# Optimization experiments

Hardware: AMD Instinct MI355X
Metric: run time of the kernel (lower is better)

## Reference

```python
import jax, jax.numpy as jnp
import numpy as np

B, N, DIM, H = 8, 4096, 768, 12
HD = DIM // H
SCALE = HD ** -0.5


def setup_inputs() -> dict:
    key = jax.random.key(0)
    ks = jax.random.split(key, 6)
    x = jax.random.normal(ks[0], (B, N, DIM), dtype=jnp.float32)
    # torch nn.Linear weights: [out_features, in_features]
    Wqkv = jax.random.normal(ks[1], (3 * DIM, DIM), dtype=jnp.float32) * (DIM ** -0.5)
    Wp = jax.random.normal(ks[2], (DIM, DIM), dtype=jnp.float32) * (DIM ** -0.5)
    bp = jnp.zeros((DIM,), dtype=jnp.float32)
    w_q = jax.random.normal(ks[3], (H, HD), dtype=jnp.float32)
    w_k = jax.random.normal(ks[4], (H, HD), dtype=jnp.float32)
    return {"x": x, "Wqkv": Wqkv, "Wp": Wp, "bp": bp, "w_q": w_q, "w_k": w_k}


def reference(x, Wqkv, Wp, bp, w_q, w_k):
    b, n, c = x.shape
    qkv = x @ Wqkv.T                                   # [B,N,3C]
    # rearrange 'B N (qkv H C) -> qkv B H N C'
    qkv = qkv.reshape(b, n, 3, H, HD).transpose(2, 0, 3, 1, 4)
    q, k, v = qkv[0], qkv[1], qkv[2]                   # each [B,H,N,hd]

    alpha = jnp.einsum('bhnc,hc->bhn', q, w_q) * SCALE
    alpha = jax.nn.softmax(alpha, axis=-1)             # [B,H,N]
    global_q = jnp.einsum('bhn,bhnc->bhc', alpha, q)   # [B,H,hd]

    p = global_q[:, :, None, :] * k                    # [B,H,N,hd]
    beta = jnp.einsum('bhnc,hc->bhn', p, w_k) * SCALE
    beta = jax.nn.softmax(beta, axis=-1)
    global_k = jnp.einsum('bhn,bhnc->bhc', beta, k)    # [B,H,hd]

    u = global_k[:, :, None, :] * v                    # [B,H,N,hd]
    q_flat = q.transpose(0, 2, 1, 3).reshape(b, n, c)  # 'B H N C -> B N (H C)'
    u_flat = u.transpose(0, 2, 1, 3).reshape(b, n, c)
    return u_flat @ Wp.T + bp + q_flat
```

## Files before the change

kernel.cpp:

```cpp
#include <hip/hip_runtime.h>
#include <hip/hip_bf16.h>
#include <cstdint>
#include <cstddef>

#define B_ 8
#define N_ 4096
#define DIM_ 768
#define H_ 12
#define M_ (B_*N_)
#define SCALE_ 0.125f
#define NS2 16
#define KDIM 768
#define NKT 12
#define NITER 6

typedef __attribute__((ext_vector_type(8))) short s8v;
typedef __attribute__((ext_vector_type(4))) float f4v;

__device__ inline float bf2f(unsigned short u) {
    unsigned v = ((unsigned)u) << 16;
    return __builtin_bit_cast(float, v);
}
__device__ inline unsigned short f2bf(float f) {
    unsigned u = __builtin_bit_cast(unsigned, f);
    return (unsigned short)((u + 0x7FFFu + ((u >> 16) & 1u)) >> 16);
}
__device__ inline void gload16(const void* g, void* l) {
    __builtin_amdgcn_global_load_lds(
        (const __attribute__((address_space(1))) void*)g,
        (__attribute__((address_space(3))) void*)l, 16, 0, 0);
}

#define BARX() __builtin_amdgcn_s_barrier()
#define PRIO1() __builtin_amdgcn_s_setprio(1)
#define PRIO0() __builtin_amdgcn_s_setprio(0)
#define VM4() asm volatile("s_waitcnt vmcnt(4)" ::: "memory")
#define VM0() asm volatile("s_waitcnt vmcnt(0)" ::: "memory")

__global__ __launch_bounds__(512, 2)
void gemm8(const unsigned short* __restrict__ A, int ldaE,
           const unsigned short* __restrict__ Bmat,
           unsigned short* __restrict__ Cb,
           const unsigned short* __restrict__ avecb,
           float* __restrict__ pv1, float* __restrict__ pms1,
           int ntn)
{
    __shared__ __align__(16) char smem[131072];
    const int tid = threadIdx.x;
    const int l = tid & 63, w = tid >> 6;
    const int lr = l & 15, g = l >> 4;
    const int wm = w >> 2, wn = w & 3;

    const int nwg = gridDim.x, cpx = nwg >> 3;
    const int bid = blockIdx.x;
    const int lg = (bid & 7) * cpx + (bid >> 3);
    const int tm = lg / ntn, tn = lg % ntn;
    const int m0 = tm * 256, n0 = tn * 256;

    const long ldaB = (long)ldaE * 2;
    const long ldbB = (long)KDIM * 2;

    const int srA = w * 8 + (l >> 3);
    const int kbs = (l & 7) * 16;
    const int kbx = kbs ^ ((srA & 7) << 4);
    long offA[2], offB[2];
    offA[0] = (long)(srA) * ldaB + kbx;
    offA[1] = (long)(128 + srA) * ldaB + kbx;
    offB[0] = (long)(((srA >> 5)) * 64 + (srA & 31)) * ldbB + kbx;
    offB[1] = (long)((2 + (srA >> 5)) * 64 + (srA & 31)) * ldbB + kbx;

    const char* Abase = (const char*)(A + (size_t)m0 * ldaE);
    const char* Bbase = (const char*)(Bmat + (size_t)n0 * KDIM);

    const int aoff = (wm * 64 + lr) * 128;
    const int boff = (wn * 32 + lr) * 128;
    const int kx0 = (g * 16) ^ ((lr & 7) << 4);
    const int kx1 = (64 + g * 16) ^ ((lr & 7) << 4);

#define STG_A(buf_, qm_, kt_) { \
    const char* s0_ = Abase + (long)(kt_) * 2 + (long)(qm_) * 64 * ldaB; \
    char* d0_ = smem + ((buf_) * 4 + (qm_)) * 16384 + w * 1024; \
    gload16(s0_ + offA[0], d0_); \
    gload16(s0_ + offA[1], d0_ + 8192); }

#define STG_B(buf_, qn_, kt_) { \
    const char* s0_ = Bbase + (long)(kt_) * 2 + (long)(qn_) * 32 * ldbB; \
    char* d0_ = smem + ((buf_) * 4 + 2 + (qn_)) * 16384 + w * 1024; \
    gload16(s0_ + offB[0], d0_); \
    gload16(s0_ + offB[1], d0_ + 8192); }

    if (tn < 3) {
        f4v acc[8][4] = {};
        s8v af[4][2];
        s8v bfr[2][2][2];

#define DS_A(buf_, qm_) { \
    const char* ba_ = smem + ((buf_) * 4 + (qm_)) * 16384 + aoff; \
    af[0][0] = *(const s8v*)(ba_ +    0 + kx0); af[0][1] = *(const s8v*)(ba_ +    0 + kx1); \
    af[1][0] = *(const s8v*)(ba_ + 2048 + kx0); af[1][1] = *(const s8v*)(ba_ + 2048 + kx1); \
    af[2][0] = *(const s8v*)(ba_ + 4096 + kx0); af[2][1] = *(const s8v*)(ba_ + 4096 + kx1); \
    af[3][0] = *(const s8v*)(ba_ + 6144 + kx0); af[3][1] = *(const s8v*)(ba_ + 6144 + kx1); }

#define DS_B(buf_, qn_) { \
    const char* bb_ = smem + ((buf_) * 4 + 2 + (qn_)) * 16384 + boff; \
    bfr[qn_][0][0] = *(const s8v*)(bb_ +    0 + kx0); bfr[qn_][0][1] = *(const s8v*)(bb_ +    0 + kx1); \
    bfr[qn_][1][0] = *(const s8v*)(bb_ + 2048 + kx0); bfr[qn_][1][1] = *(const s8v*)(bb_ + 2048 + kx1); }

#define MM(fmg_, fng_, qn_, kk_) \
    acc[fmg_][fng_] = __builtin_amdgcn_mfma_f32_16x16x32_bf16(af[(fmg_)&3][kk_], bfr[qn_][(fng_)&1][kk_], acc[fmg_][fng_], 0, 0, 0);

#define MFMA8(qm_, qn_, kk_) \
    MM((qm_)*4+0, (qn_)*2+0, qn_, kk_) MM((qm_)*4+0, (qn_)*2+1, qn_, kk_) \
    MM((qm_)*4+1, (qn_)*2+0, qn_, kk_) MM((qm_)*4+1, (qn_)*2+1, qn_, kk_) \
    MM((qm_)*4+2, (qn_)*2+0, qn_, kk_) MM((qm_)*4+2, (qn_)*2+1, qn_, kk_) \
    MM((qm_)*4+3, (qn_)*2+0, qn_, kk_) MM((qm_)*4+3, (qn_)*2+1, qn_, kk_)

#define MFMA16(qm_, qn_) { MFMA8(qm_, qn_, 0) MFMA8(qm_, qn_, 1) }

        STG_A(0, 0, 0); STG_B(0, 0, 0); STG_A(0, 1, 0); STG_B(0, 1, 0);
        STG_A(1, 0, 64); STG_B(1, 0, 64);
        VM4(); BARX();

        for (int i = 0; i < NITER; ++i) {
            const int t1k = (2 * i + 1) * 64, t2k = (2 * i + 2) * 64, t3k = (2 * i + 3) * 64;
            const bool h2 = (2 * i + 2) < NKT, h3 = (2 * i + 3) < NKT;
            const bool last = (i == NITER - 1);
            DS_A(0, 0); DS_B(0, 0); STG_B(1, 1, t1k);
            BARX(); PRIO1(); MFMA16(0, 0); PRIO0(); BARX();
            DS_B(0, 1); STG_A(1, 1, t1k);
            BARX(); PRIO1(); MFMA16(0, 1); PRIO0(); BARX();
            DS_A(0, 1); if (h2) STG_A(0, 0, t2k);
            BARX(); PRIO1(); MFMA16(1, 0); PRIO0(); BARX();
            if (h2) STG_B(0, 0, t2k);
            BARX(); PRIO1(); MFMA16(1, 1); PRIO0();
            if (last) { VM0(); } else { VM4(); }
            BARX();
            DS_A(1, 0); DS_B(1, 0); if (h2) STG_A(0, 1, t2k);
            BARX(); PRIO1(); MFMA16(0, 0); PRIO0(); BARX();
            DS_B(1, 1); if (h2) STG_B(0, 1, t2k);
            BARX(); PRIO1(); MFMA16(0, 1); PRIO0(); BARX();
            DS_A(1, 1); if (h3) STG_A(1, 0, t3k);
            BARX(); PRIO1(); MFMA16(1, 0); PRIO0(); BARX();
            if (h3) STG_B(1, 0, t3k);
            BARX(); PRIO1(); MFMA16(1, 1); PRIO0();
            if (last) { VM0(); } else { VM4(); }
            BARX();
        }

        const int c0 = tn * 256;
#pragma unroll
        for (int fmg = 0; fmg < 8; ++fmg) {
#pragma unroll
            for (int fng = 0; fng < 4; ++fng) {
                const int col = c0 + wn * 64 + fng * 16 + lr;
#pragma unroll
                for (int r = 0; r < 4; ++r) {
                    const int row = m0 + wm * 128 + fmg * 16 + g * 4 + r;
                    Cb[(size_t)row * DIM_ + col] = f2bf(acc[fmg][fng][r]);
                }
            }
        }
#undef DS_A
#undef DS_B
#undef MM
#undef MFMA8
#undef MFMA16
    } else {
        const int b = m0 >> 12;
        const int slice = (m0 & (N_ - 1)) >> 8;
        if (w < 2) {
            const int rw = l >> 3;
            const int by = ((l & 7) * 16) ^ (rw << 4);
#pragma unroll
            for (int k6 = 0; k6 < 6; ++k6) {
                const int kt = w * 6 + k6;
                gload16((const char*)avecb + (size_t)rw * 1536 + kt * 128 + by,
                        smem + 32768 + kt * 2048);
                gload16((const char*)avecb + (size_t)(8 + rw) * 1536 + kt * 128 + by,
                        smem + 32768 + kt * 2048 + 1024);
            }
        }
        STG_A(0, 0, 0); STG_A(0, 1, 0);
        STG_A(1, 0, 64); STG_A(1, 1, 64);
        VM4(); BARX();

        f4v sacc[2] = {};
        for (int kt = 0; kt < 12; ++kt) {
            const int buf = kt & 1;
#pragma unroll
            for (int j = 0; j < 2; ++j) {
                const int r0 = w * 32 + j * 16;
                const int qm = (r0 >> 6) & 1, hi = r0 >> 7, loc = r0 & 63;
                const char* ab = smem + (buf * 4 + qm) * 16384 + hi * 8192 + (loc + lr) * 128;
                s8v a0 = *(const s8v*)(ab + kx0);
                s8v a1 = *(const s8v*)(ab + kx1);
                const char* vb = smem + 32768 + kt * 2048 + lr * 128;
                s8v b0 = *(const s8v*)(vb + kx0);
                s8v b1 = *(const s8v*)(vb + kx1);
                sacc[j] = __builtin_amdgcn_mfma_f32_16x16x32_bf16(a0, b0, sacc[j], 0, 0, 0);
                sacc[j] = __builtin_amdgcn_mfma_f32_16x16x32_bf16(a1, b1, sacc[j], 0, 0, 0);
            }
            BARX();
            if (kt + 2 < 12) {
                const int kk2 = (kt + 2) * 64;
                STG_A(buf, 0, kk2); STG_A(buf, 1, kk2);
            }
            if (kt <= 9) { VM4(); } else { VM0(); }
            BARX();
        }

        float dd[8];
#pragma unroll
        for (int j = 0; j < 2; ++j)
#pragma unroll
            for (int r = 0; r < 4; ++r) dd[j * 4 + r] = sacc[j][r] * SCALE_;

        float mw = dd[0];
#pragma unroll
        for (int q2 = 1; q2 < 8; ++q2) mw = fmaxf(mw, dd[q2]);
        mw = fmaxf(mw, __shfl_xor(mw, 16));
        mw = fmaxf(mw, __shfl_xor(mw, 32));
        float* Lm = (float*)(smem + 107008);
        float* Ls = (float*)(smem + 107520);
        if (l < 16) Lm[w * 16 + lr] = mw;
        __syncthreads();
        float mfin = Lm[lr];
#pragma unroll
        for (int w2 = 1; w2 < 8; ++w2) mfin = fmaxf(mfin, Lm[w2 * 16 + lr]);

        float ss = 0.f;
#pragma unroll
        for (int j = 0; j < 2; ++j)
#pragma unroll
            for (int r = 0; r < 4; ++r) {
                const float e = __expf(dd[j * 4 + r] - mfin);
                ss += e;
                const int row = w * 32 + j * 16 + g * 4 + r;
                *(unsigned short*)(smem + 98304 + lr * 544 + row * 2) = f2bf(e);
            }
        ss += __shfl_xor(ss, 16);
        ss += __shfl_xor(ss, 32);
        if (l < 16) Ls[w * 16 + lr] = ss;
        __syncthreads();

        if (tid < 12) {
            float S = 0.f;
#pragma unroll
            for (int w2 = 0; w2 < 8; ++w2) S += Ls[w2 * 16 + tid];
            float M2 = Lm[tid];
#pragma unroll
            for (int w2 = 1; w2 < 8; ++w2) M2 = fmaxf(M2, Lm[w2 * 16 + tid]);
            pms1[((size_t)(b * H_ + tid) * 16 + slice) * 2 + 0] = M2;
            pms1[((size_t)(b * H_ + tid) * 16 + slice) * 2 + 1] = S;
        }
        __syncthreads();

        for (int it = 0; it < 6; ++it) {
            const int ktA = it * 2, ktB = it * 2 + 1;
            STG_A(0, 0, ktA * 64); STG_A(0, 1, ktA * 64);
            STG_A(1, 0, ktB * 64); STG_A(1, 1, ktB * 64);
            VM0(); BARX();
            const int buf = w >> 2;
            const int kt = it * 2 + buf;
            const int d0 = (w & 3) * 16;
            const int dby = (d0 + (l & 15)) * 2;
            f4v pacc = {};
#pragma unroll
            for (int c = 0; c < 8; ++c) {
                s8v ae = *(const s8v*)(smem + 98304 + (l & 15) * 544
                                       + (c * 32 + (l >> 4) * 8) * 2);
                const char* xr = smem + (buf * 4 + ((c >> 1) & 1)) * 16384 + (c >> 2) * 8192;
                const int nb = (c & 1) * 32 + (l >> 4) * 8;
                s8v bx;
#pragma unroll
                for (int j = 0; j < 8; ++j)
                    bx[j] = (short)*(const unsigned short*)(xr + (nb + j) * 128 + (dby ^ (j << 4)));
                pacc = __builtin_amdgcn_mfma_f32_16x16x32_bf16(ae, bx, pacc, 0, 0, 0);
            }
            if ((l >> 4) < 3) {
#pragma unroll
                for (int r = 0; r < 4; ++r) {
                    const int h = (l >> 4) * 4 + r;
                    pv1[((size_t)(b * 16 + slice) * 12 + h) * 768
                        + kt * 64 + d0 + (l & 15)] = pacc[r];
                }
            }
            BARX();
        }
    }
#undef STG_A
#undef STG_B
}

template<int MODE>
__global__ __launch_bounds__(512, 2)
void gemm128(const unsigned short* __restrict__ A, int ldaE,
             const unsigned short* __restrict__ Bmat,
             float* __restrict__ Cf, unsigned short* __restrict__ CbO,
             const float* __restrict__ bias, const float* __restrict__ addW,
             int Nc, int ntn)
{
    __shared__ __align__(16) char smem[98304];
    const int tid = threadIdx.x;
    const int l = tid & 63, w = tid >> 6;
    const int lr = l & 15, g = l >> 4;
    const int wm = w >> 2, wn = w & 3;

    const int nwg = gridDim.x, cpx = nwg >> 3;
    const int bid = blockIdx.x;
    const int lg = (bid & 7) * cpx + (bid >> 3);
    const int tm = lg / ntn, tn = lg % ntn;
    const int m0 = tm * 128, n0 = tn * 256;

    const long ldaB = (long)ldaE * 2;
    const long ldbB = (long)KDIM * 2;

    const unsigned short* Bp = Bmat;
    if (MODE == 0) Bp = Bmat + (size_t)(m0 >> 12) * (DIM_ * DIM_);

    const int srA = w * 8 + (l >> 3);
    const int kbs = (l & 7) * 16;
    const int kbx = kbs ^ ((srA & 7) << 4);
    long offA[2], offB[2];
    offA[0] = (long)(srA) * ldaB + kbx;
    offA[1] = (long)(64 + srA) * ldaB + kbx;
    offB[0] = (long)(((srA >> 5)) * 64 + (srA & 31)) * ldbB + kbx;
    offB[1] = (long)((2 + (srA >> 5)) * 64 + (srA & 31)) * ldbB + kbx;

    const char* Abase = (const char*)(A + (size_t)m0 * ldaE);
    const char* Bbase = (const char*)(Bp + (size_t)n0 * KDIM);

    const int aoff = (wm * 64 + lr) * 128;
    const int boff = (wn * 32 + lr) * 128;
    const int kx0 = (g * 16) ^ ((lr & 7) << 4);
    const int kx1 = (64 + g * 16) ^ ((lr & 7) << 4);

    f4v acc[4][4] = {};
    s8v af[4][2];
    s8v bfr[2][2][2];

#define STG_A1(buf_, kt_) { \
    const char* s0_ = Abase + (long)(kt_) * 2; \
    char* d0_ = smem + ((buf_) * 3) * 16384 + w * 1024; \
    gload16(s0_ + offA[0], d0_); \
    gload16(s0_ + offA[1], d0_ + 8192); }

#define STG_B1(buf_, qn_, kt_) { \
    const char* s0_ = Bbase + (long)(kt_) * 2 + (long)(qn_) * 32 * ldbB; \
    char* d0_ = smem + ((buf_) * 3 + 1 + (qn_)) * 16384 + w * 1024; \
    gload16(s0_ + offB[0], d0_); \
    gload16(s0_ + offB[1], d0_ + 8192); }

#define DS_A1(buf_) { \
    const char* ba_ = smem + ((buf_) * 3) * 16384 + aoff; \
    af[0][0] = *(const s8v*)(ba_ +    0 + kx0); af[0][1] = *(const s8v*)(ba_ +    0 + kx1); \
    af[1][0] = *(const s8v*)(ba_ + 2048 + kx0); af[1][1] = *(const s8v*)(ba_ + 2048 + kx1); \
    af[2][0] = *(const s8v*)(ba_ + 4096 + kx0); af[2][1] = *(const s8v*)(ba_ + 4096 + kx1); \
    af[3][0] = *(const s8v*)(ba_ + 6144 + kx0); af[3][1] = *(const s8v*)(ba_ + 6144 + kx1); }

#define DS_B1(buf_, qn_) { \
    const char* bb_ = smem + ((buf_) * 3 + 1 + (qn_)) * 16384 + boff; \
    bfr[qn_][0][0] = *(const s8v*)(bb_ +    0 + kx0); bfr[qn_][0][1] = *(const s8v*)(bb_ +    0 + kx1); \
    bfr[qn_][1][0] = *(const s8v*)(bb_ + 2048 + kx0); bfr[qn_][1][1] = *(const s8v*)(bb_ + 2048 + kx1); }

#define MM1(fm_, fng_, qn_, kk_) \
    acc[fm_][fng_] = __builtin_amdgcn_mfma_f32_16x16x32_bf16(af[fm_][kk_], bfr[qn_][(fng_)&1][kk_], acc[fm_][fng_], 0, 0, 0);

#define MFMA16_1(qn_, kk_) \
    MM1(0, (qn_)*2+0, qn_, kk_) MM1(0, (qn_)*2+1, qn_, kk_) \
    MM1(1, (qn_)*2+0, qn_, kk_) MM1(1, (qn_)*2+1, qn_, kk_) \
    MM1(2, (qn_)*2+0, qn_, kk_) MM1(2, (qn_)*2+1, qn_, kk_) \
    MM1(3, (qn_)*2+0, qn_, kk_) MM1(3, (qn_)*2+1, qn_, kk_)

#define MFMA32_1(qn_) { MFMA16_1(qn_, 0) MFMA16_1(qn_, 1) }

    STG_A1(0, 0); STG_B1(0, 0, 0); STG_B1(0, 1, 0);
    STG_A1(1, 64); STG_B1(1, 0, 64);
    VM4(); BARX();

    for (int i = 0; i < NITER; ++i) {
        const int t1k = (2 * i + 1) * 64, t2k = (2 * i + 2) * 64, t3k = (2 * i + 3) * 64;
        const bool h2 = (2 * i + 2) < NKT, h3 = (2 * i + 3) < NKT;
        const bool last = (i == NITER - 1);
        DS_A1(0); DS_B1(0, 0); STG_B1(1, 1, t1k);
        BARX(); PRIO1(); MFMA32_1(0); PRIO0(); BARX();
        DS_B1(0, 1); if (h2) { STG_A1(0, t2k); STG_B1(0, 0, t2k); }
        BARX(); PRIO1(); MFMA32_1(1); PRIO0();
        if (last) { VM0(); } else { VM4(); }
        BARX();
        DS_A1(1); DS_B1(1, 0); if (h2) STG_B1(0, 1, t2k);
        BARX(); PRIO1(); MFMA32_1(0); PRIO0(); BARX();
        DS_B1(1, 1); if (h3) { STG_A1(1, t3k); STG_B1(1, 0, t3k); }
        BARX(); PRIO1(); MFMA32_1(1); PRIO0();
        if (last) { VM0(); } else { VM4(); }
        BARX();
    }

    const int jb = m0 % DIM_;
#pragma unroll
    for (int fm = 0; fm < 4; ++fm) {
#pragma unroll
        for (int fng = 0; fng < 4; ++fng) {
            const int col = n0 + wn * 64 + fng * 16 + lr;
#pragma unroll
            for (int r = 0; r < 4; ++r) {
                const int ro = wm * 64 + fm * 16 + g * 4 + r;
                const int row = m0 + ro;
                if (MODE == 0) {
                    Cf[(size_t)row * Nc + col] = acc[fm][fng][r] + bias[col];
                } else {
                    CbO[(size_t)row * Nc + col] =
                        f2bf(acc[fm][fng][r] + addW[(size_t)(jb + ro) * DIM_ + col]);
                }
            }
        }
    }
#undef STG_A1
#undef STG_B1
#undef DS_A1
#undef DS_B1
#undef MM1
#undef MFMA16_1
#undef MFMA32_1
}

__global__ __launch_bounds__(256)
void reduce_a(const float* __restrict__ pv1, const float* __restrict__ pms1,
              const float* __restrict__ Wqkv, const float* __restrict__ w_k,
              float* __restrict__ gqwk)
{
    const int b = blockIdx.x / H_, h = blockIdx.x % H_;
    const int t = threadIdx.x;
    const int w = t >> 6, l = t & 63;
    __shared__ float Svec[768];
    __shared__ float ew[16];
    __shared__ float Ssh;

    const float* pp = pms1 + (size_t)(b * H_ + h) * 16 * 2;
    float M = pp[0];
    for (int s = 1; s < 16; ++s) M = fmaxf(M, pp[s * 2]);
    if (t < 16) ew[t] = __expf(pp[t * 2] - M);
    __syncthreads();
    if (t == 0) {
        float S = 0.f;
        for (int s = 0; s < 16; ++s) S += ew[s] * pp[s * 2 + 1];
        Ssh = S;
    }
#pragma unroll
    for (int j = 0; j < 3; ++j) {
        const int col = t + j * 256;
        float v = 0.f;
        for (int s = 0; s < 16; ++s)
            v += ew[s] * pv1[((size_t)(b * 16 + s) * 12 + h) * 768 + col];
        Svec[col] = v;
    }
    __syncthreads();

    const float invS = 1.f / Ssh;
    for (int i = 0; i < 16; ++i) {
        const int o = w * 16 + i;
        const float* wr = Wqkv + (size_t)(h * 64 + o) * 768;
        float s = 0.f;
#pragma unroll
        for (int j = 0; j < 12; ++j)
            s += wr[l + j * 64] * Svec[l + j * 64];
        s += __shfl_xor(s, 1); s += __shfl_xor(s, 2); s += __shfl_xor(s, 4);
        s += __shfl_xor(s, 8); s += __shfl_xor(s, 16); s += __shfl_xor(s, 32);
        if (l == 0)
            gqwk[(size_t)(b * H_ + h) * 64 + o] = (s * invS) * w_k[h * 64 + o];
    }
}

__global__ __launch_bounds__(256)
void fused_b(const unsigned short* __restrict__ kb,
             const float* __restrict__ gqwk,
             float* __restrict__ pv2, float* __restrict__ pms2)
{
    const int bid = blockIdx.x;
    const int bh = bid / NS2, sp = bid % NS2;
    const int b = bh / H_, h = bh % H_;
    const int t = threadIdx.x;
    const int lane8 = t & 7, grp = t >> 3;

    __shared__ float gq_s[64];
    if (t < 64) gq_s[t] = gqwk[(size_t)bh * 64 + t];
    __syncthreads();

    float w8[8];
#pragma unroll
    for (int j = 0; j < 8; j++) w8[j] = gq_s[lane8 * 8 + j];

    const unsigned short* base = kb + ((size_t)(b * N_ + sp * 256) * DIM_)
                                 + h * 64 + lane8 * 8;
    float q[8][8];
    float d[8];
#pragma unroll
    for (int pass = 0; pass < 8; ++pass) {
        const int row = pass * 32 + grp;
        s8v q8 = *(const s8v*)(base + (size_t)row * DIM_);
        float s = 0.f;
#pragma unroll
        for (int j = 0; j < 8; j++) {
            q[pass][j] = bf2f((unsigned short)q8[j]);
            s += q[pass][j] * w8[j];
        }
        s += __shfl_xor(s, 1); s += __shfl_xor(s, 2); s += __shfl_xor(s, 4);
        d[pass] = s * SCALE_;
    }
    float m = d[0];
#pragma unroll
    for (int pass = 1; pass < 8; ++pass) m = fmaxf(m, d[pass]);
    float ssum = 0.f;
    float a8[8] = {};
#pragma unroll
    for (int pass = 0; pass < 8; ++pass) {
        float e = __expf(d[pass] - m);
        ssum += e;
#pragma unroll
        for (int j = 0; j < 8; j++) a8[j] += e * q[pass][j];
    }

    __shared__ float Lm[32], Ls[32];
    __shared__ float La[32][64];
    if (lane8 == 0) { Lm[grp] = m; Ls[grp] = ssum; }
#pragma unroll
    for (int j = 0; j < 8; j++) La[grp][lane8 * 8 + j] = a8[j];
    __syncthreads();

    if (t < 64) {
        float mstar = Lm[0];
#pragma unroll
        for (int g2 = 1; g2 < 32; ++g2) mstar = fmaxf(mstar, Lm[g2]);
        float sstar = 0.f, v = 0.f;
#pragma unroll
        for (int g2 = 0; g2 < 32; ++g2) {
            float e = __expf(Lm[g2] - mstar);
            sstar += Ls[g2] * e;
            v += La[g2][t] * e;
        }
        pv2[(size_t)bid * 64 + t] = v;
        if (t == 0) { pms2[bid * 2] = mstar; pms2[bid * 2 + 1] = sstar; }
    }
}

__global__ void path_reduce(const float* __restrict__ partv, const float* __restrict__ partms,
                            int nsp, float* __restrict__ gout)
{
    const int bh = blockIdx.x;
    const int t = threadIdx.x;
    float mstar = partms[(bh * nsp) * 2];
    for (int p = 1; p < nsp; ++p) mstar = fmaxf(mstar, partms[(bh * nsp + p) * 2]);
    float sstar = 0.f, v = 0.f;
    for (int p = 0; p < nsp; ++p) {
        float e = __expf(partms[(bh * nsp + p) * 2] - mstar);
        sstar += partms[(bh * nsp + p) * 2 + 1] * e;
        v += partv[(size_t)(bh * nsp + p) * 64 + t] * e;
    }
    gout[bh * 64 + t] = v / sstar;
}

__global__ __launch_bounds__(256)
void avec_prep(const float* __restrict__ Wqkv, const float* __restrict__ w_q,
               unsigned short* __restrict__ avecb)
{
    const int h = blockIdx.x;
    const int t = threadIdx.x;
    if (h >= H_) {
#pragma unroll
        for (int j = 0; j < 3; ++j) avecb[(size_t)h * 768 + t + j * 256] = 0;
        return;
    }
    __shared__ float wl[64];
    if (t < 64) wl[t] = w_q[h * 64 + t];
    __syncthreads();
#pragma unroll
    for (int j = 0; j < 3; ++j) {
        const int dcol = t + j * 256;
        float a = 0.f;
        for (int c = 0; c < 64; ++c)
            a += wl[c] * Wqkv[(size_t)(h * 64 + c) * 768 + dcol];
        avecb[(size_t)h * 768 + dcol] = f2bf(a);
    }
}

__global__ void cvt_all(const float* __restrict__ x, const float* __restrict__ Wqkv,
                        unsigned short* __restrict__ xb, unsigned short* __restrict__ wqkb,
                        unsigned short* __restrict__ wvT,
                        int n4x, int n4xw)
{
    int i = blockIdx.x * 256 + threadIdx.x;
    if (i < n4xw) {
        const float* src; unsigned short* dst; int k;
        if (i < n4x) { src = x; dst = xb; k = i; }
        else { src = Wqkv + (size_t)DIM_ * DIM_; dst = wqkb; k = i - n4x; }
        float4 v = ((const float4*)src)[k];
        ushort4 o;
        o.x = f2bf(v.x); o.y = f2bf(v.y); o.z = f2bf(v.z); o.w = f2bf(v.w);
        ((ushort4*)dst)[k] = o;
    } else {
        const int k = i - n4xw;
        const int ii = k % DIM_;
        const int c0 = (k / DIM_) * 4;
        ushort4 o;
        o.x = f2bf(Wqkv[(size_t)(2 * DIM_ + c0 + 0) * DIM_ + ii]);
        o.y = f2bf(Wqkv[(size_t)(2 * DIM_ + c0 + 1) * DIM_ + ii]);
        o.z = f2bf(Wqkv[(size_t)(2 * DIM_ + c0 + 2) * DIM_ + ii]);
        o.w = f2bf(Wqkv[(size_t)(2 * DIM_ + c0 + 3) * DIM_ + ii]);
        *(ushort4*)&wvT[(size_t)ii * DIM_ + c0] = o;
    }
}

__global__ __launch_bounds__(256)
void fold_wp(const float* __restrict__ Wp, const float* __restrict__ gk,
             unsigned short* __restrict__ W2)
{
    int idx = blockIdx.x * 256 + threadIdx.x;
    int e4 = idx * 4;
    int b = (int)((unsigned)e4 / (unsigned)(DIM_ * DIM_));
    int rem = e4 - b * (DIM_ * DIM_);
    int c = rem % DIM_;
    float4 wv = *(const float4*)&Wp[rem];
    const float* gp = &gk[b * DIM_ + c];
    ushort4 o;
    o.x = f2bf(wv.x * gp[0]); o.y = f2bf(wv.y * gp[1]);
    o.z = f2bf(wv.z * gp[2]); o.w = f2bf(wv.w * gp[3]);
    *(ushort4*)&W2[e4] = o;
}

extern "C" void kernel_launch(void* const* d_in, const int* in_sizes, int n_in,
                              void* d_out, int out_size, void* d_ws, size_t ws_size,
                              hipStream_t stream)
{
    const float* x    = (const float*)d_in[0];
    const float* Wqkv = (const float*)d_in[1];
    const float* Wp   = (const float*)d_in[2];
    const float* bp   = (const float*)d_in[3];
    const float* w_q  = (const float*)d_in[4];
    const float* w_k  = (const float*)d_in[5];
    float* out = (float*)d_out;

    constexpr size_t NXB = (size_t)M_ * DIM_;
    constexpr size_t NWK = (size_t)DIM_ * DIM_;
    constexpr size_t NWV = (size_t)DIM_ * DIM_;
    constexpr size_t NKB = (size_t)M_ * DIM_;
    constexpr size_t NW2 = (size_t)B_ * DIM_ * DIM_;

    char* p = (char*)d_ws;
    unsigned short* xb    = (unsigned short*)p; p += NXB * 2;
    unsigned short* wqkb  = (unsigned short*)p; p += NWK * 2;
    unsigned short* wvT   = (unsigned short*)p; p += NWV * 2;
    unsigned short* kb    = (unsigned short*)p; p += NKB * 2;
    unsigned short* w2b   = (unsigned short*)p; p += NW2 * 2;
    unsigned short* w4b   = (unsigned short*)p; p += NW2 * 2;
    unsigned short* avecb = (unsigned short*)p; p += (size_t)16 * 768 * 2;
    float* pv1  = (float*)p; p += (size_t)B_ * 16 * 12 * 768 * 4;
    float* pms1 = (float*)p; p += (size_t)B_ * H_ * 16 * 2 * 4;
    float* pv2  = (float*)p; p += (size_t)B_ * H_ * NS2 * 64 * 4;
    float* pms2 = (float*)p; p += (size_t)B_ * H_ * NS2 * 2 * 4;
    float* gqwk = (float*)p; p += (size_t)B_ * H_ * 64 * 4;
    float* gkv  = (float*)p; p += (size_t)B_ * H_ * 64 * 4;

    constexpr int N4X  = (int)(NXB / 4);
    constexpr int N4XW = N4X + (int)(NWK / 4);
    constexpr int NTOT = N4XW + (int)(NWV / 4);
    cvt_all<<<NTOT / 256, 256, 0, stream>>>(x, Wqkv, xb, wqkb, wvT, N4X, N4XW);

    avec_prep<<<16, 256, 0, stream>>>(Wqkv, w_q, avecb);

    gemm8<<<128 * 4, 512, 0, stream>>>(xb, DIM_, wqkb, kb, avecb, pv1, pms1, 4);

    reduce_a<<<B_ * H_, 256, 0, stream>>>(pv1, pms1, Wqkv, w_k, gqwk);

    fused_b<<<B_ * H_ * NS2, 256, 0, stream>>>(kb, gqwk, pv2, pms2);
    path_reduce<<<B_ * H_, 64, 0, stream>>>(pv2, pms2, NS2, gkv);

    fold_wp<<<(int)(NW2 / 4 / 256), 256, 0, stream>>>(Wp, gkv, w2b);

    gemm128<1><<<48 * 3, 512, 0, stream>>>(w2b, DIM_, wvT, nullptr, w4b, nullptr, Wqkv,
                                           DIM_, 3);

    gemm128<0><<<256 * 3, 512, 0, stream>>>(xb, DIM_, w4b, out, nullptr, bp, nullptr,
                                            DIM_, 3);
}
```

Measured before the change: 209.5 us.

## Fold K projection into second score pass instead of materializing K

Drops the full x@Wk GEMM that wrote K to memory. The beta scores are instead computed as x dotted with per-batch folded vectors (gq*w_k)·Wk, reusing the same score_pass kernel used for alpha, followed by a reduce that projects the x-weighted sum back through Wk. This removes a large GEMM and the K write and read traffic. The cost is a second streaming pass over x and extra per-head reduction work in reduce_a and reduce_b.

```diff
diff --git a/kernel.cpp b/kernel.cpp
--- a/kernel.cpp
+++ b/kernel.cpp
@@ -9,7 +9,6 @@
 #define H_ 12
 #define M_ (B_*N_)
 #define SCALE_ 0.125f
-#define NS2 16
 #define KDIM 768
 #define NKT 12
 #define NITER 6
@@ -37,43 +36,35 @@
 #define VM4() asm volatile("s_waitcnt vmcnt(4)" ::: "memory")
 #define VM0() asm volatile("s_waitcnt vmcnt(0)" ::: "memory")
 
+template<int PATH>
 __global__ __launch_bounds__(512, 2)
-void gemm8(const unsigned short* __restrict__ A, int ldaE,
-           const unsigned short* __restrict__ Bmat,
-           unsigned short* __restrict__ Cb,
-           const unsigned short* __restrict__ avecb,
-           float* __restrict__ pv1, float* __restrict__ pms1,
-           int ntn)
-{
-    __shared__ __align__(16) char smem[131072];
+void score_pass(const unsigned short* __restrict__ xb,
+                const unsigned short* __restrict__ Vmat,
+                float* __restrict__ pv, float* __restrict__ pms)
+{
+    __shared__ __align__(16) char smem[110592];
     const int tid = threadIdx.x;
     const int l = tid & 63, w = tid >> 6;
     const int lr = l & 15, g = l >> 4;
-    const int wm = w >> 2, wn = w & 3;
 
     const int nwg = gridDim.x, cpx = nwg >> 3;
     const int bid = blockIdx.x;
-    const int lg = (bid & 7) * cpx + (bid >> 3);
-    const int tm = lg / ntn, tn = lg % ntn;
-    const int m0 = tm * 256, n0 = tn * 256;
-
-    const long ldaB = (long)ldaE * 2;
-    const long ldbB = (long)KDIM * 2;
-
+    const int tm = (bid & 7) * cpx + (bid >> 3);
+    const int m0 = tm * 256;
+    const int b = m0 >> 12;
+    const int slice = (m0 & (N_ - 1)) >> 8;
+
+    const long ldaB = (long)KDIM * 2;
     const int srA = w * 8 + (l >> 3);
     const int kbs = (l & 7) * 16;
     const int kbx = kbs ^ ((srA & 7) << 4);
-    long offA[2], offB[2];
+    long offA[2];
     offA[0] = (long)(srA) * ldaB + kbx;
     offA[1] = (long)(128 + srA) * ldaB + kbx;
-    offB[0] = (long)(((srA >> 5)) * 64 + (srA & 31)) * ldbB + kbx;
-    offB[1] = (long)((2 + (srA >> 5)) * 64 + (srA & 31)) * ldbB + kbx;
-
-    const char* Abase = (const char*)(A + (size_t)m0 * ldaE);
-    const char* Bbase = (const char*)(Bmat + (size_t)n0 * KDIM);
-
-    const int aoff = (wm * 64 + lr) * 128;
-    const int boff = (wn * 32 + lr) * 128;
+
+    const char* Abase = (const char*)(xb + (size_t)m0 * KDIM);
+    const char* Vbase = (const char*)Vmat + (PATH ? (size_t)b * 16 * KDIM * 2 : 0);
+
     const int kx0 = (g * 16) ^ ((lr & 7) << 4);
     const int kx1 = (64 + g * 16) ^ ((lr & 7) << 4);
 
@@ -83,213 +74,126 @@
     gload16(s0_ + offA[0], d0_); \
     gload16(s0_ + offA[1], d0_ + 8192); }
 
-#define STG_B(buf_, qn_, kt_) { \
-    const char* s0_ = Bbase + (long)(kt_) * 2 + (long)(qn_) * 32 * ldbB; \
-    char* d0_ = smem + ((buf_) * 4 + 2 + (qn_)) * 16384 + w * 1024; \
-    gload16(s0_ + offB[0], d0_); \
-    gload16(s0_ + offB[1], d0_ + 8192); }
-
-    if (tn < 3) {
-        f4v acc[8][4] = {};
-        s8v af[4][2];
-        s8v bfr[2][2][2];
-
-#define DS_A(buf_, qm_) { \
-    const char* ba_ = smem + ((buf_) * 4 + (qm_)) * 16384 + aoff; \
-    af[0][0] = *(const s8v*)(ba_ +    0 + kx0); af[0][1] = *(const s8v*)(ba_ +    0 + kx1); \
-    af[1][0] = *(const s8v*)(ba_ + 2048 + kx0); af[1][1] = *(const s8v*)(ba_ + 2048 + kx1); \
-    af[2][0] = *(const s8v*)(ba_ + 4096 + kx0); af[2][1] = *(const s8v*)(ba_ + 4096 + kx1); \
-    af[3][0] = *(const s8v*)(ba_ + 6144 + kx0); af[3][1] = *(const s8v*)(ba_ + 6144 + kx1); }
-
-#define DS_B(buf_, qn_) { \
-    const char* bb_ = smem + ((buf_) * 4 + 2 + (qn_)) * 16384 + boff; \
-    bfr[qn_][0][0] = *(const s8v*)(bb_ +    0 + kx0); bfr[qn_][0][1] = *(const s8v*)(bb_ +    0 + kx1); \
-    bfr[qn_][1][0] = *(const s8v*)(bb_ + 2048 + kx0); bfr[qn_][1][1] = *(const s8v*)(bb_ + 2048 + kx1); }
-
-#define MM(fmg_, fng_, qn_, kk_) \
-    acc[fmg_][fng_] = __builtin_amdgcn_mfma_f32_16x16x32_bf16(af[(fmg_)&3][kk_], bfr[qn_][(fng_)&1][kk_], acc[fmg_][fng_], 0, 0, 0);
-
-#define MFMA8(qm_, qn_, kk_) \
-    MM((qm_)*4+0, (qn_)*2+0, qn_, kk_) MM((qm_)*4+0, (qn_)*2+1, qn_, kk_) \
-    MM((qm_)*4+1, (qn_)*2+0, qn_, kk_) MM((qm_)*4+1, (qn_)*2+1, qn_, kk_) \
-    MM((qm_)*4+2, (qn_)*2+0, qn_, kk_) MM((qm_)*4+2, (qn_)*2+1, qn_, kk_) \
-    MM((qm_)*4+3, (qn_)*2+0, qn_, kk_) MM((qm_)*4+3, (qn_)*2+1, qn_, kk_)
-
-#define MFMA16(qm_, qn_) { MFMA8(qm_, qn_, 0) MFMA8(qm_, qn_, 1) }
-
-        STG_A(0, 0, 0); STG_B(0, 0, 0); STG_A(0, 1, 0); STG_B(0, 1, 0);
-        STG_A(1, 0, 64); STG_B(1, 0, 64);
-        VM4(); BARX();
-
-        for (int i = 0; i < NITER; ++i) {
-            const int t1k = (2 * i + 1) * 64, t2k = (2 * i + 2) * 64, t3k = (2 * i + 3) * 64;
-            const bool h2 = (2 * i + 2) < NKT, h3 = (2 * i + 3) < NKT;
-            const bool last = (i == NITER - 1);
-            DS_A(0, 0); DS_B(0, 0); STG_B(1, 1, t1k);
-            BARX(); PRIO1(); MFMA16(0, 0); PRIO0(); BARX();
-            DS_B(0, 1); STG_A(1, 1, t1k);
-            BARX(); PRIO1(); MFMA16(0, 1); PRIO0(); BARX();
-            DS_A(0, 1); if (h2) STG_A(0, 0, t2k);
-            BARX(); PRIO1(); MFMA16(1, 0); PRIO0(); BARX();
-            if (h2) STG_B(0, 0, t2k);
-            BARX(); PRIO1(); MFMA16(1, 1); PRIO0();
-            if (last) { VM0(); } else { VM4(); }
-            BARX();
-            DS_A(1, 0); DS_B(1, 0); if (h2) STG_A(0, 1, t2k);
-            BARX(); PRIO1(); MFMA16(0, 0); PRIO0(); BARX();
-            DS_B(1, 1); if (h2) STG_B(0, 1, t2k);
-            BARX(); PRIO1(); MFMA16(0, 1); PRIO0(); BARX();
-            DS_A(1, 1); if (h3) STG_A(1, 0, t3k);
-            BARX(); PRIO1(); MFMA16(1, 0); PRIO0(); BARX();
-            if (h3) STG_B(1, 0, t3k);
-            BARX(); PRIO1(); MFMA16(1, 1); PRIO0();
-            if (last) { VM0(); } else { VM4(); }
-            BARX();
-        }
-
-        const int c0 = tn * 256;
-#pragma unroll
-        for (int fmg = 0; fmg < 8; ++fmg) {
-#pragma unroll
-            for (int fng = 0; fng < 4; ++fng) {
-                const int col = c0 + wn * 64 + fng * 16 + lr;
-#pragma unroll
-                for (int r = 0; r < 4; ++r) {
-                    const int row = m0 + wm * 128 + fmg * 16 + g * 4 + r;
-                    Cb[(size_t)row * DIM_ + col] = f2bf(acc[fmg][fng][r]);
-                }
+    if (w < 2) {
+        const int rw = l >> 3;
+        const int by = ((l & 7) * 16) ^ (rw << 4);
+#pragma unroll
+        for (int k6 = 0; k6 < 6; ++k6) {
+            const int kt = w * 6 + k6;
+            gload16(Vbase + (size_t)rw * 1536 + kt * 128 + by,
+                    smem + 32768 + kt * 2048);
+            gload16(Vbase + (size_t)(8 + rw) * 1536 + kt * 128 + by,
+                    smem + 32768 + kt * 2048 + 1024);
+        }
+    }
+    STG_A(0, 0, 0); STG_A(0, 1, 0);
+    STG_A(1, 0, 64); STG_A(1, 1, 64);
+    VM4(); BARX();
+
+    f4v sacc[2] = {};
+    for (int kt = 0; kt < 12; ++kt) {
+        const int buf = kt & 1;
+#pragma unroll
+        for (int j = 0; j < 2; ++j) {
+            const int r0 = w * 32 + j * 16;
+            const int qm = (r0 >> 6) & 1, hi = r0 >> 7, loc = r0 & 63;
+            const char* ab = smem + (buf * 4 + qm) * 16384 + hi * 8192 + (loc + lr) * 128;
+            s8v a0 = *(const s8v*)(ab + kx0);
+            s8v a1 = *(const s8v*)(ab + kx1);
+            const char* vb = smem + 32768 + kt * 2048 + lr * 128;
+            s8v b0 = *(const s8v*)(vb + kx0);
+            s8v b1 = *(const s8v*)(vb + kx1);
+            sacc[j] = __builtin_amdgcn_mfma_f32_16x16x32_bf16(a0, b0, sacc[j], 0, 0, 0);
+            sacc[j] = __builtin_amdgcn_mfma_f32_16x16x32_bf16(a1, b1, sacc[j], 0, 0, 0);
+        }
+        BARX();
+        if (kt + 2 < 12) {
+            const int kk2 = (kt + 2) * 64;
+            STG_A(buf, 0, kk2); STG_A(buf, 1, kk2);
+        }
+        if (kt <= 9) { VM4(); } else { VM0(); }
+        BARX();
+    }
+
+    float dd[8];
+#pragma unroll
+    for (int j = 0; j < 2; ++j)
+#pragma unroll
+        for (int r = 0; r < 4; ++r) dd[j * 4 + r] = sacc[j][r] * SCALE_;
+
+    float mw = dd[0];
+#pragma unroll
+    for (int q2 = 1; q2 < 8; ++q2) mw = fmaxf(mw, dd[q2]);
+    mw = fmaxf(mw, __shfl_xor(mw, 16));
+    mw = fmaxf(mw, __shfl_xor(mw, 32));
+    float* Lm = (float*)(smem + 107008);
+    float* Ls = (float*)(smem + 107520);
+    if (l < 16) Lm[w * 16 + lr] = mw;
+    __syncthreads();
+    float mfin = Lm[lr];
+#pragma unroll
+    for (int w2 = 1; w2 < 8; ++w2) mfin = fmaxf(mfin, Lm[w2 * 16 + lr]);
+
+    float ss = 0.f;
+#pragma unroll
+    for (int j = 0; j < 2; ++j)
+#pragma unroll
+        for (int r = 0; r < 4; ++r) {
+            const float e = __expf(dd[j * 4 + r] - mfin);
+            ss += e;
+            const int row = w * 32 + j * 16 + g * 4 + r;
+            *(unsigned short*)(smem + 98304 + lr * 544 + row * 2) = f2bf(e);
+        }
+    ss += __shfl_xor(ss, 16);
+    ss += __shfl_xor(ss, 32);
+    if (l < 16) Ls[w * 16 + lr] = ss;
+    __syncthreads();
+
+    if (tid < 12) {
+        float S = 0.f;
+#pragma unroll
+        for (int w2 = 0; w2 < 8; ++w2) S += Ls[w2 * 16 + tid];
+        float M2 = Lm[tid];
+#pragma unroll
+        for (int w2 = 1; w2 < 8; ++w2) M2 = fmaxf(M2, Lm[w2 * 16 + tid]);
+        pms[((size_t)(b * H_ + tid) * 16 + slice) * 2 + 0] = M2;
+        pms[((size_t)(b * H_ + tid) * 16 + slice) * 2 + 1] = S;
+    }
+    __syncthreads();
+
+    for (int it = 0; it < 6; ++it) {
+        const int ktA = it * 2, ktB = it * 2 + 1;
+        STG_A(0, 0, ktA * 64); STG_A(0, 1, ktA * 64);
+        STG_A(1, 0, ktB * 64); STG_A(1, 1, ktB * 64);
+        VM0(); BARX();
+        const int buf = w >> 2;
+        const int kt = it * 2 + buf;
+        const int d0 = (w & 3) * 16;
+        const int dby = (d0 + (l & 15)) * 2;
+        f4v pacc = {};
+#pragma unroll
+        for (int c = 0; c < 8; ++c) {
+            s8v ae = *(const s8v*)(smem + 98304 + (l & 15) * 544
+                                   + (c * 32 + (l >> 4) * 8) * 2);
+            const char* xr = smem + (buf * 4 + ((c >> 1) & 1)) * 16384 + (c >> 2) * 8192;
+            const int nb = (c & 1) * 32 + (l >> 4) * 8;
+            s8v bx;
+#pragma unroll
+            for (int j = 0; j < 8; ++j)
+                bx[j] = (short)*(const unsigned short*)(xr + (nb + j) * 128 + (dby ^ (j << 4)));
+            pacc = __builtin_amdgcn_mfma_f32_16x16x32_bf16(ae, bx, pacc, 0, 0, 0);
+        }
+        if ((l >> 4) < 3) {
+#pragma unroll
+            for (int r = 0; r < 4; ++r) {
+                const int h = (l >> 4) * 4 + r;
+                pv[((size_t)(b * 16 + slice) * 12 + h) * 768
+                   + kt * 64 + d0 + (l & 15)] = pacc[r];
             }
         }
-#undef DS_A
-#undef DS_B
-#undef MM
-#undef MFMA8
-#undef MFMA16
-    } else {
-        const int b = m0 >> 12;
-        const int slice = (m0 & (N_ - 1)) >> 8;
-        if (w < 2) {
-            const int rw = l >> 3;
-            const int by = ((l & 7) * 16) ^ (rw << 4);
-#pragma unroll
-            for (int k6 = 0; k6 < 6; ++k6) {
-                const int kt = w * 6 + k6;
-                gload16((const char*)avecb + (size_t)rw * 1536 + kt * 128 + by,
-                        smem + 32768 + kt * 2048);
-                gload16((const char*)avecb + (size_t)(8 + rw) * 1536 + kt * 128 + by,
-                        smem + 32768 + kt * 2048 + 1024);
-            }
-        }
-        STG_A(0, 0, 0); STG_A(0, 1, 0);
-        STG_A(1, 0, 64); STG_A(1, 1, 64);
-        VM4(); BARX();
-
-        f4v sacc[2] = {};
-        for (int kt = 0; kt < 12; ++kt) {
-            const int buf = kt & 1;
-#pragma unroll
-            for (int j = 0; j < 2; ++j) {
-                const int r0 = w * 32 + j * 16;
-                const int qm = (r0 >> 6) & 1, hi = r0 >> 7, loc = r0 & 63;
-                const char* ab = smem + (buf * 4 + qm) * 16384 + hi * 8192 + (loc + lr) * 128;
-                s8v a0 = *(const s8v*)(ab + kx0);
-                s8v a1 = *(const s8v*)(ab + kx1);
-                const char* vb = smem + 32768 + kt * 2048 + lr * 128;
-                s8v b0 = *(const s8v*)(vb + kx0);
-                s8v b1 = *(const s8v*)(vb + kx1);
-                sacc[j] = __builtin_amdgcn_mfma_f32_16x16x32_bf16(a0, b0, sacc[j], 0, 0, 0);
-                sacc[j] = __builtin_amdgcn_mfma_f32_16x16x32_bf16(a1, b1, sacc[j], 0, 0, 0);
-            }
-            BARX();
-            if (kt + 2 < 12) {
-                const int kk2 = (kt + 2) * 64;
-                STG_A(buf, 0, kk2); STG_A(buf, 1, kk2);
-            }
-            if (kt <= 9) { VM4(); } else { VM0(); }
-            BARX();
-        }
-
-        float dd[8];
-#pragma unroll
-        for (int j = 0; j < 2; ++j)
-#pragma unroll
-            for (int r = 0; r < 4; ++r) dd[j * 4 + r] = sacc[j][r] * SCALE_;
-
-        float mw = dd[0];
-#pragma unroll
-        for (int q2 = 1; q2 < 8; ++q2) mw = fmaxf(mw, dd[q2]);
-        mw = fmaxf(mw, __shfl_xor(mw, 16));
-        mw = fmaxf(mw, __shfl_xor(mw, 32));
-        float* Lm = (float*)(smem + 107008);
-        float* Ls = (float*)(smem + 107520);
-        if (l < 16) Lm[w * 16 + lr] = mw;
-        __syncthreads();
-        float mfin = Lm[lr];
-#pragma unroll
-        for (int w2 = 1; w2 < 8; ++w2) mfin = fmaxf(mfin, Lm[w2 * 16 + lr]);
-
-        float ss = 0.f;
-#pragma unroll
-        for (int j = 0; j < 2; ++j)
-#pragma unroll
-            for (int r = 0; r < 4; ++r) {
-                const float e = __expf(dd[j * 4 + r] - mfin);
-                ss += e;
-                const int row = w * 32 + j * 16 + g * 4 + r;
-                *(unsigned short*)(smem + 98304 + lr * 544 + row * 2) = f2bf(e);
-            }
-        ss += __shfl_xor(ss, 16);
-        ss += __shfl_xor(ss, 32);
-        if (l < 16) Ls[w * 16 + lr] = ss;
-        __syncthreads();
-
-        if (tid < 12) {
-            float S = 0.f;
-#pragma unroll
-            for (int w2 = 0; w2 < 8; ++w2) S += Ls[w2 * 16 + tid];
-            float M2 = Lm[tid];
-#pragma unroll
-            for (int w2 = 1; w2 < 8; ++w2) M2 = fmaxf(M2, Lm[w2 * 16 + tid]);
-            pms1[((size_t)(b * H_ + tid) * 16 + slice) * 2 + 0] = M2;
-            pms1[((size_t)(b * H_ + tid) * 16 + slice) * 2 + 1] = S;
-        }
-        __syncthreads();
-
-        for (int it = 0; it < 6; ++it) {
-            const int ktA = it * 2, ktB = it * 2 + 1;
-            STG_A(0, 0, ktA * 64); STG_A(0, 1, ktA * 64);
-            STG_A(1, 0, ktB * 64); STG_A(1, 1, ktB * 64);
-            VM0(); BARX();
-            const int buf = w >> 2;
-            const int kt = it * 2 + buf;
-            const int d0 = (w & 3) * 16;
-            const int dby = (d0 + (l & 15)) * 2;
-            f4v pacc = {};
-#pragma unroll
-            for (int c = 0; c < 8; ++c) {
-                s8v ae = *(const s8v*)(smem + 98304 + (l & 15) * 544
-                                       + (c * 32 + (l >> 4) * 8) * 2);
-                const char* xr = smem + (buf * 4 + ((c >> 1) & 1)) * 16384 + (c >> 2) * 8192;
-                const int nb = (c & 1) * 32 + (l >> 4) * 8;
-                s8v bx;
-#pragma unroll
-                for (int j = 0; j < 8; ++j)
-                    bx[j] = (short)*(const unsigned short*)(xr + (nb + j) * 128 + (dby ^ (j << 4)));
-                pacc = __builtin_amdgcn_mfma_f32_16x16x32_bf16(ae, bx, pacc, 0, 0, 0);
-            }
-            if ((l >> 4) < 3) {
-#pragma unroll
-                for (int r = 0; r < 4; ++r) {
-                    const int h = (l >> 4) * 4 + r;
-                    pv1[((size_t)(b * 16 + slice) * 12 + h) * 768
-                        + kt * 64 + d0 + (l & 15)] = pacc[r];
-                }
-            }
-            BARX();
-        }
+        BARX();
     }
 #undef STG_A
-#undef STG_B
 }
 
 template<int MODE>
@@ -427,7 +331,7 @@
 __global__ __launch_bounds__(256)
 void reduce_a(const float* __restrict__ pv1, const float* __restrict__ pms1,
               const float* __restrict__ Wqkv, const float* __restrict__ w_k,
-              float* __restrict__ gqwk)
+              unsigned short* __restrict__ bvecs)
 {
     const int b = blockIdx.x / H_, h = blockIdx.x % H_;
     const int t = threadIdx.x;
@@ -435,6 +339,7 @@
     __shared__ float Svec[768];
     __shared__ float ew[16];
     __shared__ float Ssh;
+    __shared__ float gqwk[64];
 
     const float* pp = pms1 + (size_t)(b * H_ + h) * 16 * 2;
     float M = pp[0];
@@ -466,97 +371,64 @@
             s += wr[l + j * 64] * Svec[l + j * 64];
         s += __shfl_xor(s, 1); s += __shfl_xor(s, 2); s += __shfl_xor(s, 4);
         s += __shfl_xor(s, 8); s += __shfl_xor(s, 16); s += __shfl_xor(s, 32);
-        if (l == 0)
-            gqwk[(size_t)(b * H_ + h) * 64 + o] = (s * invS) * w_k[h * 64 + o];
+        if (l == 0) gqwk[o] = (s * invS) * w_k[h * 64 + o];
+    }
+    __syncthreads();
+
+#pragma unroll
+    for (int j = 0; j < 3; ++j) {
+        const int dcol = t + j * 256;
+        float bv = 0.f;
+        for (int c = 0; c < 64; ++c)
+            bv += gqwk[c] * Wqkv[(size_t)(DIM_ + h * 64 + c) * 768 + dcol];
+        bvecs[(size_t)(b * 16 + h) * 768 + dcol] = f2bf(bv);
+        if (h < 4) bvecs[(size_t)(b * 16 + 12 + h) * 768 + dcol] = 0;
     }
 }
 
 __global__ __launch_bounds__(256)
-void fused_b(const unsigned short* __restrict__ kb,
-             const float* __restrict__ gqwk,
-             float* __restrict__ pv2, float* __restrict__ pms2)
-{
-    const int bid = blockIdx.x;
-    const int bh = bid / NS2, sp = bid % NS2;
-    const int b = bh / H_, h = bh % H_;
+void reduce_b(const float* __restrict__ pv2, const float* __restrict__ pms2,
+              const float* __restrict__ Wqkv, float* __restrict__ gkv)
+{
+    const int b = blockIdx.x / H_, h = blockIdx.x % H_;
     const int t = threadIdx.x;
-    const int lane8 = t & 7, grp = t >> 3;
-
-    __shared__ float gq_s[64];
-    if (t < 64) gq_s[t] = gqwk[(size_t)bh * 64 + t];
-    __syncthreads();
-
-    float w8[8];
-#pragma unroll
-    for (int j = 0; j < 8; j++) w8[j] = gq_s[lane8 * 8 + j];
-
-    const unsigned short* base = kb + ((size_t)(b * N_ + sp * 256) * DIM_)
-                                 + h * 64 + lane8 * 8;
-    float q[8][8];
-    float d[8];
-#pragma unroll
-    for (int pass = 0; pass < 8; ++pass) {
-        const int row = pass * 32 + grp;
-        s8v q8 = *(const s8v*)(base + (size_t)row * DIM_);
+    const int w = t >> 6, l = t & 63;
+    __shared__ float Svec[768];
+    __shared__ float ew[16];
+    __shared__ float Ssh;
+
+    const float* pp = pms2 + (size_t)(b * H_ + h) * 16 * 2;
+    float M = pp[0];
+    for (int s = 1; s < 16; ++s) M = fmaxf(M, pp[s * 2]);
+    if (t < 16) ew[t] = __expf(pp[t * 2] - M);
+    __syncthreads();
+    if (t == 0) {
+        float S = 0.f;
+        for (int s = 0; s < 16; ++s) S += ew[s] * pp[s * 2 + 1];
+        Ssh = S;
+    }
+#pragma unroll
+    for (int j = 0; j < 3; ++j) {
+        const int col = t + j * 256;
+        float v = 0.f;
+        for (int s = 0; s < 16; ++s)
+            v += ew[s] * pv2[((size_t)(b * 16 + s) * 12 + h) * 768 + col];
+        Svec[col] = v;
+    }
+    __syncthreads();
+
+    const float invS = 1.f / Ssh;
+    for (int i = 0; i < 16; ++i) {
+        const int o = w * 16 + i;
+        const float* wr = Wqkv + (size_t)(DIM_ + h * 64 + o) * 768;
         float s = 0.f;
 #pragma unroll
-        for (int j = 0; j < 8; j++) {
-            q[pass][j] = bf2f((unsigned short)q8[j]);
-            s += q[pass][j] * w8[j];
-        }
+        for (int j = 0; j < 12; ++j)
+            s += wr[l + j * 64] * Svec[l + j * 64];
         s += __shfl_xor(s, 1); s += __shfl_xor(s, 2); s += __shfl_xor(s, 4);
-        d[pass] = s * SCALE_;
-    }
-    float m = d[0];
-#pragma unroll
-    for (int pass = 1; pass < 8; ++pass) m = fmaxf(m, d[pass]);
-    float ssum = 0.f;
-    float a8[8] = {};
-#pragma unroll
-    for (int pass = 0; pass < 8; ++pass) {
-        float e = __expf(d[pass] - m);
-        ssum += e;
-#pragma unroll
-        for (int j = 0; j < 8; j++) a8[j] += e * q[pass][j];
-    }
-
-    __shared__ float Lm[32], Ls[32];
-    __shared__ float La[32][64];
-    if (lane8 == 0) { Lm[grp] = m; Ls[grp] = ssum; }
-#pragma unroll
-    for (int j = 0; j < 8; j++) La[grp][lane8 * 8 + j] = a8[j];
-    __syncthreads();
-
-    if (t < 64) {
-        float mstar = Lm[0];
-#pragma unroll
-        for (int g2 = 1; g2 < 32; ++g2) mstar = fmaxf(mstar, Lm[g2]);
-        float sstar = 0.f, v = 0.f;
-#pragma unroll
-        for (int g2 = 0; g2 < 32; ++g2) {
-            float e = __expf(Lm[g2] - mstar);
-            sstar += Ls[g2] * e;
-            v += La[g2][t] * e;
-        }
-        pv2[(size_t)bid * 64 + t] = v;
-        if (t == 0) { pms2[bid * 2] = mstar; pms2[bid * 2 + 1] = sstar; }
-    }
-}
-
-__global__ void path_reduce(const float* __restrict__ partv, const float* __restrict__ partms,
-                            int nsp, float* __restrict__ gout)
-{
-    const int bh = blockIdx.x;
-    const int t = threadIdx.x;
-    float mstar = partms[(bh * nsp) * 2];
-    for (int p = 1; p < nsp; ++p) mstar = fmaxf(mstar, partms[(bh * nsp + p) * 2]);
-    float sstar = 0.f, v = 0.f;
-    for (int p = 0; p < nsp; ++p) {
-        float e = __expf(partms[(bh * nsp + p) * 2] - mstar);
-        sstar += partms[(bh * nsp + p) * 2 + 1] * e;
-        v += partv[(size_t)(bh * nsp + p) * 64 + t] * e;
-    }
-    gout[bh * 64 + t] = v / sstar;
+        s += __shfl_xor(s, 8); s += __shfl_xor(s, 16); s += __shfl_xor(s, 32);
+        if (l == 0) gkv[(size_t)b * DIM_ + h * 64 + o] = s * invS;
+    }
 }
 
 __global__ __launch_bounds__(256)
@@ -584,21 +456,17 @@
 }
 
 __global__ void cvt_all(const float* __restrict__ x, const float* __restrict__ Wqkv,
-                        unsigned short* __restrict__ xb, unsigned short* __restrict__ wqkb,
-                        unsigned short* __restrict__ wvT,
-                        int n4x, int n4xw)
+                        unsigned short* __restrict__ xb, unsigned short* __restrict__ wvT,
+                        int n4x)
 {
     int i = blockIdx.x * 256 + threadIdx.x;
-    if (i < n4xw) {
-        const float* src; unsigned short* dst; int k;
-        if (i < n4x) { src = x; dst = xb; k = i; }
-        else { src = Wqkv + (size_t)DIM_ * DIM_; dst = wqkb; k = i - n4x; }
-        float4 v = ((const float4*)src)[k];
+    if (i < n4x) {
+        float4 v = ((const float4*)x)[i];
         ushort4 o;
         o.x = f2bf(v.x); o.y = f2bf(v.y); o.z = f2bf(v.z); o.w = f2bf(v.w);
-        ((ushort4*)dst)[k] = o;
+        ((ushort4*)xb)[i] = o;
     } else {
-        const int k = i - n4xw;
+        const int k = i - n4x;
         const int ii = k % DIM_;
         const int c0 = (k / DIM_) * 4;
         ushort4 o;
@@ -640,39 +508,35 @@
     float* out = (float*)d_out;
 
     constexpr size_t NXB = (size_t)M_ * DIM_;
-    constexpr size_t NWK = (size_t)DIM_ * DIM_;
     constexpr size_t NWV = (size_t)DIM_ * DIM_;
-    constexpr size_t NKB = (size_t)M_ * DIM_;
     constexpr size_t NW2 = (size_t)B_ * DIM_ * DIM_;
 
     char* p = (char*)d_ws;
     unsigned short* xb    = (unsigned short*)p; p += NXB * 2;
-    unsigned short* wqkb  = (unsigned short*)p; p += NWK * 2;
     unsigned short* wvT   = (unsigned short*)p; p += NWV * 2;
-    unsigned short* kb    = (unsigned short*)p; p += NKB * 2;
     unsigned short* w2b   = (unsigned short*)p; p += NW2 * 2;
     unsigned short* w4b   = (unsigned short*)p; p += NW2 * 2;
     unsigned short* avecb = (unsigned short*)p; p += (size_t)16 * 768 * 2;
+    unsigned short* bvecs = (unsigned short*)p; p += (size_t)B_ * 16 * 768 * 2;
     float* pv1  = (float*)p; p += (size_t)B_ * 16 * 12 * 768 * 4;
     float* pms1 = (float*)p; p += (size_t)B_ * H_ * 16 * 2 * 4;
-    float* pv2  = (float*)p; p += (size_t)B_ * H_ * NS2 * 64 * 4;
-    float* pms2 = (float*)p; p += (size_t)B_ * H_ * NS2 * 2 * 4;
-    float* gqwk = (float*)p; p += (size_t)B_ * H_ * 64 * 4;
-    float* gkv  = (float*)p; p += (size_t)B_ * H_ * 64 * 4;
+    float* pv2  = (float*)p; p += (size_t)B_ * 16 * 12 * 768 * 4;
+    float* pms2 = (float*)p; p += (size_t)B_ * H_ * 16 * 2 * 4;
+    float* gkv  = (float*)p; p += (size_t)B_ * DIM_ * 4;
 
     constexpr int N4X  = (int)(NXB / 4);
-    constexpr int N4XW = N4X + (int)(NWK / 4);
-    constexpr int NTOT = N4XW + (int)(NWV / 4);
-    cvt_all<<<NTOT / 256, 256, 0, stream>>>(x, Wqkv, xb, wqkb, wvT, N4X, N4XW);
+    constexpr int NTOT = N4X + (int)(NWV / 4);
+    cvt_all<<<NTOT / 256, 256, 0, stream>>>(x, Wqkv, xb, wvT, N4X);
 
     avec_prep<<<16, 256, 0, stream>>>(Wqkv, w_q, avecb);
 
-    gemm8<<<128 * 4, 512, 0, stream>>>(xb, DIM_, wqkb, kb, avecb, pv1, pms1, 4);
-
-    reduce_a<<<B_ * H_, 256, 0, stream>>>(pv1, pms1, Wqkv, w_k, gqwk);
-
-    fused_b<<<B_ * H_ * NS2, 256, 0, stream>>>(kb, gqwk, pv2, pms2);
-    path_reduce<<<B_ * H_, 64, 0, stream>>>(pv2, pms2, NS2, gkv);
+    score_pass<0><<<128, 512, 0, stream>>>(xb, avecb, pv1, pms1);
+
+    reduce_a<<<B_ * H_, 256, 0, stream>>>(pv1, pms1, Wqkv, w_k, bvecs);
+
+    score_pass<1><<<128, 512, 0, stream>>>(xb, bvecs, pv2, pms2);
+
+    reduce_b<<<B_ * H_, 256, 0, stream>>>(pv2, pms2, Wqkv, gkv);
 
     fold_wp<<<(int)(NW2 / 4 / 256), 256, 0, stream>>>(Wp, gkv, w2b);
 
```

New measurement: 199.9 us. 1.05x faster.
